# Optimization experiments

Hardware: AMD Instinct MI355X
Metric: run time of the kernel (lower is better)

## Reference

```python
import jax, jax.numpy as jnp
import numpy as np

F_TOT = 108
OUT_CH = 5
GNN_IN = 5


def setup_inputs() -> dict:
    key = jax.random.key(0)
    ks = jax.random.split(key, 24)
    B, S, N, E = 16, 1, 20000, 320000
    s = 0.1  # param init scale
    d = {}
    d["x"] = jax.random.normal(ks[0], (B, S, N, F_TOT), jnp.float32)
    d["edge_index"] = jax.random.randint(ks[1], (2, E), 0, N, dtype=jnp.int32)
    # four Conv1d(1, 5, k=24) branches
    for i, nm in enumerate(["t", "r", "tp", "ssr"]):
        d[f"w_{nm}"] = s * jax.random.normal(ks[2 + 2 * i], (OUT_CH, 1, 24), jnp.float32)
        d[f"b_{nm}"] = s * jax.random.normal(ks[3 + 2 * i], (OUT_CH,), jnp.float32)
    # fc1: 32 -> 20, fc2: 20 -> 5
    d["fc1_w"] = s * jax.random.normal(ks[10], (20, 12 + 4 * OUT_CH), jnp.float32)
    d["fc1_b"] = s * jax.random.normal(ks[11], (20,), jnp.float32)
    d["fc2_w"] = s * jax.random.normal(ks[12], (GNN_IN, 20), jnp.float32)
    d["fc2_b"] = s * jax.random.normal(ks[13], (GNN_IN,), jnp.float32)
    # SAGEConv(5 -> 20): lin_l (with bias, applied to mean-aggregated neighbors), lin_r (no bias, root)
    d["g1_wl"] = s * jax.random.normal(ks[14], (20, GNN_IN), jnp.float32)
    d["g1_bl"] = s * jax.random.normal(ks[15], (20,), jnp.float32)
    d["g1_wr"] = s * jax.random.normal(ks[16], (20, GNN_IN), jnp.float32)
    # SAGEConv(20 -> 1)
    d["g2_wl"] = s * jax.random.normal(ks[17], (1, 20), jnp.float32)
    d["g2_bl"] = s * jax.random.normal(ks[18], (1,), jnp.float32)
    d["g2_wr"] = s * jax.random.normal(ks[19], (1, 20), jnp.float32)
    return d


def _branch(xs, w, b):
    # Conv1d(in=1, out=5, k=24) over a length-24 window == a single dot product per channel.
    # xs: [NB, 24], w: [5, 1, 24] -> [NB, 5], then ReLU
    return jax.nn.relu(jnp.einsum('nk,ok->no', xs, w[:, 0, :]) + b)


def _sage(h, src, dst, wl, bl, wr, n_nodes):
    # PyG SAGEConv with mean aggregation: out = lin_l(mean_{j in N(i)} x_j) + lin_r(x_i)
    # h: [B, N, d]
    msg = jnp.transpose(h[:, src, :], (1, 0, 2))                    # [E, B, d]
    agg = jax.ops.segment_sum(msg, dst, num_segments=n_nodes)       # [N, B, d]
    deg = jax.ops.segment_sum(jnp.ones((src.shape[0],), h.dtype), dst, num_segments=n_nodes)
    mean = jnp.transpose(agg, (1, 0, 2)) / jnp.maximum(deg, 1.0)[None, :, None]  # [B, N, d]
    return mean @ wl.T + bl + h @ wr.T


def reference(x, edge_index, w_t, b_t, w_r, b_r, w_tp, b_tp, w_ssr, b_ssr,
              fc1_w, fc1_b, fc2_w, fc2_b, g1_wl, g1_bl, g1_wr, g2_wl, g2_bl, g2_wr):
    B, S, N, F = x.shape
    src, dst = edge_index[0], edge_index[1]
    # permute(2,0,1,3).reshape(N*B, S, F); S == 1
    xs = jnp.transpose(x, (2, 0, 1, 3)).reshape(N * B, S, F)[:, 0, :]  # [NB, 108]
    out_t = _branch(xs[:, 12:36], w_t, b_t)
    out_r = _branch(xs[:, 36:60], w_r, b_r)
    out_tp = _branch(xs[:, 60:84], w_tp, b_tp)
    out_ssr = _branch(xs[:, 84:108], w_ssr, b_ssr)
    feat = jnp.concatenate([xs[:, :12], out_t, out_r, out_tp, out_ssr], axis=1)  # [NB, 32]
    h = jax.nn.relu(feat @ fc1_w.T + fc1_b) @ fc2_w.T + fc2_b                    # [NB, 5]
    h = jnp.transpose(h.reshape(N, B, -1), (1, 0, 2))                            # [B, N, 5]
    h = _sage(h, src, dst, g1_wl, g1_bl, g1_wr, N)                               # [B, N, 20]
    h = _sage(h, src, dst, g2_wl, g2_bl, g2_wr, N)                               # [B, N, 1]
    return jnp.transpose(h, (0, 2, 1))                                           # [B, 1, N]
```

## Files before the change

kernel.cpp:

```cpp
#include <hip/hip_runtime.h>


#define F1W 500
#define F1B 1160
#define CO  1180
#define FEAT 1266
#define HL   3378

__global__ void k_zero(int* __restrict__ cnt, int N) {
  int n = blockIdx.x * blockDim.x + threadIdx.x;
  if (n < N) cnt[n] = 0;
}

__global__ void k_count(const int* __restrict__ dst, int E, int* __restrict__ cnt) {
  int e = blockIdx.x * blockDim.x + threadIdx.x;
  if (e < E) atomicAdd(&cnt[dst[e]], 1);
}

__global__ __launch_bounds__(1024) void k_scan(
    const int* __restrict__ cnt, int N,
    int* __restrict__ row_ptr, int* __restrict__ cursor,
    const float* __restrict__ f2w, const float* __restrict__ f2b,
    const float* __restrict__ g1_wl, const float* __restrict__ g1_bl,
    const float* __restrict__ g1_wr, const float* __restrict__ g2_wl,
    const float* __restrict__ g2_wr, float* __restrict__ coef) {
  int t = threadIdx.x;

  if (t < 21) {
    float a[5], r1[5], c[5], r2[5];
#pragma unroll
    for (int k = 0; k < 5; ++k) { a[k] = 0.f; r1[k] = 0.f; c[k] = 0.f; r2[k] = 0.f; }
#pragma unroll
    for (int j = 0; j < 20; ++j) {
      float wl2 = g2_wl[j], wr2 = g2_wr[j];
#pragma unroll
      for (int k = 0; k < 5; ++k) {
        float wl1 = g1_wl[j * 5 + k], wr1 = g1_wr[j * 5 + k];
        a[k]  = fmaf(wl2, wl1, a[k]);
        r1[k] = fmaf(wr2, wl1, r1[k]);
        c[k]  = fmaf(wl2, wr1, c[k]);
        r2[k] = fmaf(wr2, wr1, r2[k]);
      }
    }
    if (t < 20) {
      float A = 0.f, R1 = 0.f, C = 0.f, R2 = 0.f;
#pragma unroll
      for (int k = 0; k < 5; ++k) {
        float w = f2w[k * 20 + t];
        A  = fmaf(a[k],  w, A);
        R1 = fmaf(r1[k], w, R1);
        C  = fmaf(c[k],  w, C);
        R2 = fmaf(r2[k], w, R2);
      }
      coef[t] = A; coef[20 + t] = R1; coef[40 + t] = C; coef[60 + t] = R2;
    } else {
      float ca = 0.f, cr1 = 0.f, cc = 0.f, cr2 = 0.f;
#pragma unroll
      for (int k = 0; k < 5; ++k) {
        float b = f2b[k];
        ca = fmaf(a[k], b, ca);  cr1 = fmaf(r1[k], b, cr1);
        cc = fmaf(c[k], b, cc);  cr2 = fmaf(r2[k], b, cr2);
      }
      coef[80] = ca; coef[81] = cr1; coef[82] = cc; coef[83] = cr2;
      float kb1 = 0.f, kb2 = 0.f;
#pragma unroll
      for (int j = 0; j < 20; ++j) {
        kb1 = fmaf(g2_wl[j], g1_bl[j], kb1);
        kb2 = fmaf(g2_wr[j], g1_bl[j], kb2);
      }
      coef[84] = kb1; coef[85] = kb2;
    }
  }

  __shared__ int part[1024];
  int chunk = (N + 1023) / 1024;
  int s0 = t * chunk, s1 = min(N, s0 + chunk);
  int sum = 0;
  for (int i = s0; i < s1; ++i) sum += cnt[i];
  part[t] = sum;
  __syncthreads();
  for (int off = 1; off < 1024; off <<= 1) {
    int v = (t >= off) ? part[t - off] : 0;
    __syncthreads();
    part[t] += v;
    __syncthreads();
  }
  int run = (t == 0) ? 0 : part[t - 1];
  for (int i = s0; i < s1; ++i) {
    row_ptr[i] = run; cursor[i] = run;
    run += cnt[i];
  }
  if (s1 == N) row_ptr[N] = run;
}

__global__ void k_scatter(const int* __restrict__ src, const int* __restrict__ dst, int E,
                          int* __restrict__ cursor, int* __restrict__ adj) {
  int e = blockIdx.x * blockDim.x + threadIdx.x;
  if (e < E) {
    int pos = atomicAdd(&cursor[dst[e]], 1);
    adj[pos] = src[e];
  }
}

__global__ __launch_bounds__(256) void k_mlp(
    const float* __restrict__ x,
    const float* __restrict__ w_t, const float* __restrict__ b_t,
    const float* __restrict__ w_r, const float* __restrict__ b_r,
    const float* __restrict__ w_tp, const float* __restrict__ b_tp,
    const float* __restrict__ w_ssr, const float* __restrict__ b_ssr,
    const float* __restrict__ f1w, const float* __restrict__ f1b,
    const float* __restrict__ coef,
    float2* __restrict__ F1v, float2* __restrict__ F2v, int N, int rows) {
  __shared__ float S[4978];
  const int t = threadIdx.x;
  const int q = t & 3, r = t >> 2;
  int rr = blockIdx.x * 64 + r;
  bool live = rr < rows;
  if (!live) rr = rows - 1;

  const float4* xv = reinterpret_cast<const float4*>(x + (size_t)rr * 108);
  float4 bv[6];
#pragma unroll
  for (int i = 0; i < 6; ++i) bv[i] = xv[3 + 6 * q + i];
  float4 pv = make_float4(0.f, 0.f, 0.f, 0.f);
  if (q > 0) pv = xv[q - 1];

  if (t < 120) {
    S[t] = w_t[t]; S[120 + t] = w_r[t]; S[240 + t] = w_tp[t]; S[360 + t] = w_ssr[t];
  }
  if (t < 5) {
    S[480 + t] = b_t[t]; S[485 + t] = b_r[t];
    S[490 + t] = b_tp[t]; S[495 + t] = b_ssr[t];
  }
  for (int i = t; i < 640; i += 256) {
    int o = i >> 5, k = i & 31;
    S[F1W + o * 33 + k] = f1w[i];
  }
  if (t < 20) S[F1B + t] = f1b[t];
  if (t >= 128 && t < 128 + 86) S[CO + t - 128] = coef[t - 128];
  __syncthreads();

  float acc[5];
#pragma unroll
  for (int o = 0; o < 5; ++o) acc[o] = S[480 + q * 5 + o];
#pragma unroll
  for (int i = 0; i < 6; ++i) {
    float4 w4 = bv[i];
#pragma unroll
    for (int o = 0; o < 5; ++o) {
      const int wb = q * 120 + o * 24 + 4 * i;
      acc[o] = fmaf(w4.x, S[wb + 0], acc[o]);
      acc[o] = fmaf(w4.y, S[wb + 1], acc[o]);
      acc[o] = fmaf(w4.z, S[wb + 2], acc[o]);
      acc[o] = fmaf(w4.w, S[wb + 3], acc[o]);
    }
  }
  float* fr = &S[FEAT + r * 33];
  if (q > 0) {
    fr[4 * (q - 1) + 0] = pv.x; fr[4 * (q - 1) + 1] = pv.y;
    fr[4 * (q - 1) + 2] = pv.z; fr[4 * (q - 1) + 3] = pv.w;
  }
#pragma unroll
  for (int o = 0; o < 5; ++o) fr[12 + q * 5 + o] = fmaxf(acc[o], 0.f);
  __syncthreads();

  float a2[5];
#pragma unroll
  for (int j = 0; j < 5; ++j) a2[j] = S[F1B + q * 5 + j];
#pragma unroll
  for (int i = 0; i < 32; ++i) {
    float f = fr[i];
#pragma unroll
    for (int j = 0; j < 5; ++j)
      a2[j] = fmaf(f, S[F1W + (q * 5 + j) * 33 + i], a2[j]);
  }
  float* hr = &S[HL + r * 25];
#pragma unroll
  for (int j = 0; j < 5; ++j) hr[q * 5 + j] = fmaxf(a2[j], 0.f);
  __syncthreads();

  float s = S[CO + 80 + q];
#pragma unroll
  for (int i = 0; i < 20; ++i) s = fmaf(hr[i], S[CO + q * 20 + i], s);
  hr[20 + q] = s;
  __syncthreads();

  if (q == 0 && live) {
    int b = rr / N;
    int n = rr - b * N;
    F1v[n * 16 + b] = make_float2(hr[20], hr[21]);
    F2v[n * 16 + b] = make_float2(hr[22], hr[23]);
  }
}

__global__ void k_agg1(const int* __restrict__ row_ptr, const int* __restrict__ adj,
                       const float2* __restrict__ F1v, const float2* __restrict__ F2v,
                       float* __restrict__ W, float* __restrict__ V, int N) {
  int t = blockIdx.x * blockDim.x + threadIdx.x;
  int g = t >> 4, b = t & 15;
  if (g >= N) return;
  int beg = row_ptr[g], end = row_ptr[g + 1];
  float sa = 0.f, sb = 0.f;
  for (int c = beg; c < end; c += 16) {
    int idx = c + b;
    int a = adj[idx < end ? idx : end - 1];
    int m = min(16, end - c);
    for (int k = 0; k < m; ++k) {
      int s = __shfl(a, k, 16);
      float2 f = F1v[s * 16 + b];
      sa += f.x; sb += f.y;
    }
  }
  float inv = 1.0f / fmaxf((float)(end - beg), 1.0f);
  float2 f2 = F2v[t];
  W[t] = sa * inv + f2.x;
  V[t] = sb * inv;
}

__global__ __launch_bounds__(256) void k_agg2(
    const int* __restrict__ row_ptr, const int* __restrict__ adj,
    const float* __restrict__ W, const float* __restrict__ V,
    const float2* __restrict__ F2v, const float* __restrict__ coef,
    const float* __restrict__ g2_bl, float* __restrict__ out, int N) {
  __shared__ float tile[16][17];
  int t = blockIdx.x * 256 + threadIdx.x;
  int g = t >> 4, b = t & 15;
  float r = 0.f;
  if (g < N) {
    int beg = row_ptr[g], end = row_ptr[g + 1];
    float sw = 0.f;
    for (int c = beg; c < end; c += 16) {
      int idx = c + b;
      int a = adj[idx < end ? idx : end - 1];
      int m = min(16, end - c);
      for (int k = 0; k < m; ++k) {
        int s = __shfl(a, k, 16);
        sw += W[s * 16 + b];
      }
    }
    int deg = end - beg;
    float inv = 1.0f / fmaxf((float)deg, 1.0f);
    float chi = deg > 0 ? 1.f : 0.f;
    r = sw * inv + V[t] + F2v[t].y + coef[84] * chi + coef[85] + g2_bl[0];
  }
  int gl = (threadIdx.x >> 4);
  tile[b][gl] = r;
  __syncthreads();
  int b2 = threadIdx.x >> 4;
  int gl2 = threadIdx.x & 15;
  int n2 = blockIdx.x * 16 + gl2;
  if (n2 < N) out[(size_t)b2 * N + n2] = tile[b2][gl2];
}

extern "C" void kernel_launch(void* const* d_in, const int* in_sizes, int n_in,
                              void* d_out, int out_size, void* d_ws, size_t ws_size,
                              hipStream_t stream) {
  const float* x     = (const float*)d_in[0];
  const int*   ei    = (const int*)d_in[1];
  const float* w_t   = (const float*)d_in[2];
  const float* b_t   = (const float*)d_in[3];
  const float* w_r   = (const float*)d_in[4];
  const float* b_r   = (const float*)d_in[5];
  const float* w_tp  = (const float*)d_in[6];
  const float* b_tp  = (const float*)d_in[7];
  const float* w_ssr = (const float*)d_in[8];
  const float* b_ssr = (const float*)d_in[9];
  const float* f1w   = (const float*)d_in[10];
  const float* f1b   = (const float*)d_in[11];
  const float* f2w   = (const float*)d_in[12];
  const float* f2b   = (const float*)d_in[13];
  const float* g1_wl = (const float*)d_in[14];
  const float* g1_bl = (const float*)d_in[15];
  const float* g1_wr = (const float*)d_in[16];
  const float* g2_wl = (const float*)d_in[17];
  const float* g2_bl = (const float*)d_in[18];
  const float* g2_wr = (const float*)d_in[19];
  float* out = (float*)d_out;

  const int E = in_sizes[1] / 2;
  const int N = out_size / 16;
  const int rows = out_size;
  const int* src = ei;
  const int* dst = ei + E;

  float* ws  = (float*)d_ws;
  float2* F1v = (float2*)ws;
  float2* F2v = F1v + (size_t)16 * N;
  float*  W   = (float*)(F2v + (size_t)16 * N);
  float*  V   = W + (size_t)16 * N;
  float*  coef = V + (size_t)16 * N;
  int* cnt     = (int*)(coef + 128);
  int* row_ptr = cnt + N;
  int* cursor  = row_ptr + N + 1;
  int* adj     = cursor + N;

  int nb16 = (N * 16 + 255) / 256;

  k_zero<<<(N + 255) / 256, 256, 0, stream>>>(cnt, N);
  k_count<<<(E + 255) / 256, 256, 0, stream>>>(dst, E, cnt);
  k_scan<<<1, 1024, 0, stream>>>(cnt, N, row_ptr, cursor,
                                 f2w, f2b, g1_wl, g1_bl, g1_wr, g2_wl, g2_wr, coef);
  k_scatter<<<(E + 255) / 256, 256, 0, stream>>>(src, dst, E, cursor, adj);
  k_mlp<<<(rows + 63) / 64, 256, 0, stream>>>(
      x, w_t, b_t, w_r, b_r, w_tp, b_tp, w_ssr, b_ssr,
      f1w, f1b, coef, F1v, F2v, N, rows);
  k_agg1<<<nb16, 256, 0, stream>>>(row_ptr, adj, F1v, F2v, W, V, N);
  k_agg2<<<nb16, 256, 0, stream>>>(row_ptr, adj, W, V, F2v, coef, g2_bl, out, N);
}
```

Baseline: 145.5 us.

## Double-buffer x tiles into LDS via async global_load_lds in k_mlp

New measurement: 172.7 us. 1.19x slower.

```diff
diff --git a/kernel.cpp b/kernel.cpp
--- a/kernel.cpp
+++ b/kernel.cpp
@@ -1,11 +1,12 @@
 #include <hip/hip_runtime.h>
 
 
-#define F1W 500
-#define F1B 1160
-#define CO  1180
-#define FEAT 1266
-#define HL   3378
+#define BUF0 0
+#define BUF1 6912
+#define WB   13824
+#define FEAT 15090
+#define HL   17202
+#define LDS_TOT 18802
 
 __global__ void k_zero(int* __restrict__ cnt, int N) {
   int n = blockIdx.x * blockDim.x + threadIdx.x;
@@ -102,6 +103,23 @@
   }
 }
 
+__device__ __forceinline__ void stage_tile(const float* __restrict__ x,
+                                           float* lbuf, int row0, int rows,
+                                           int w, int lane) {
+#pragma unroll
+  for (int j = 0; j < 7; ++j) {
+    int s = j * 4 + w; if (s > 26) s = 26;
+    int c = s * 64 + lane;
+    int dr = c / 27, part = c - dr * 27;
+    int row = row0 + dr; if (row >= rows) row = rows - 1;
+    const float* src = x + (size_t)row * 108 + part * 4;
+    __builtin_amdgcn_global_load_lds(
+        (const __attribute__((address_space(1))) unsigned int*)src,
+        (__attribute__((address_space(3))) unsigned int*)(lbuf + s * 256),
+        16, 0, 0);
+  }
+}
+
 __global__ __launch_bounds__(256) void k_mlp(
     const float* __restrict__ x,
     const float* __restrict__ w_t, const float* __restrict__ b_t,
@@ -111,85 +129,103 @@
     const float* __restrict__ f1w, const float* __restrict__ f1b,
     const float* __restrict__ coef,
     float2* __restrict__ F1v, float2* __restrict__ F2v, int N, int rows) {
-  __shared__ float S[4978];
+  __shared__ float S[LDS_TOT];
   const int t = threadIdx.x;
+  const int w = t >> 6, lane = t & 63;
   const int q = t & 3, r = t >> 2;
-  int rr = blockIdx.x * 64 + r;
-  bool live = rr < rows;
-  if (!live) rr = rows - 1;
-
-  const float4* xv = reinterpret_cast<const float4*>(x + (size_t)rr * 108);
-  float4 bv[6];
-#pragma unroll
-  for (int i = 0; i < 6; ++i) bv[i] = xv[3 + 6 * q + i];
-  float4 pv = make_float4(0.f, 0.f, 0.f, 0.f);
-  if (q > 0) pv = xv[q - 1];
+  const int base = blockIdx.x * 256;
+
+  stage_tile(x, S + BUF0, base, rows, w, lane);
 
   if (t < 120) {
-    S[t] = w_t[t]; S[120 + t] = w_r[t]; S[240 + t] = w_tp[t]; S[360 + t] = w_ssr[t];
+    S[WB + t] = w_t[t]; S[WB + 120 + t] = w_r[t];
+    S[WB + 240 + t] = w_tp[t]; S[WB + 360 + t] = w_ssr[t];
   }
   if (t < 5) {
-    S[480 + t] = b_t[t]; S[485 + t] = b_r[t];
-    S[490 + t] = b_tp[t]; S[495 + t] = b_ssr[t];
+    S[WB + 480 + t] = b_t[t]; S[WB + 485 + t] = b_r[t];
+    S[WB + 490 + t] = b_tp[t]; S[WB + 495 + t] = b_ssr[t];
   }
   for (int i = t; i < 640; i += 256) {
     int o = i >> 5, k = i & 31;
-    S[F1W + o * 33 + k] = f1w[i];
-  }
-  if (t < 20) S[F1B + t] = f1b[t];
-  if (t >= 128 && t < 128 + 86) S[CO + t - 128] = coef[t - 128];
-  __syncthreads();
-
-  float acc[5];
-#pragma unroll
-  for (int o = 0; o < 5; ++o) acc[o] = S[480 + q * 5 + o];
-#pragma unroll
-  for (int i = 0; i < 6; ++i) {
-    float4 w4 = bv[i];
-#pragma unroll
-    for (int o = 0; o < 5; ++o) {
-      const int wb = q * 120 + o * 24 + 4 * i;
-      acc[o] = fmaf(w4.x, S[wb + 0], acc[o]);
-      acc[o] = fmaf(w4.y, S[wb + 1], acc[o]);
-      acc[o] = fmaf(w4.z, S[wb + 2], acc[o]);
-      acc[o] = fmaf(w4.w, S[wb + 3], acc[o]);
-    }
-  }
-  float* fr = &S[FEAT + r * 33];
-  if (q > 0) {
-    fr[4 * (q - 1) + 0] = pv.x; fr[4 * (q - 1) + 1] = pv.y;
-    fr[4 * (q - 1) + 2] = pv.z; fr[4 * (q - 1) + 3] = pv.w;
-  }
-#pragma unroll
-  for (int o = 0; o < 5; ++o) fr[12 + q * 5 + o] = fmaxf(acc[o], 0.f);
-  __syncthreads();
-
-  float a2[5];
-#pragma unroll
-  for (int j = 0; j < 5; ++j) a2[j] = S[F1B + q * 5 + j];
-#pragma unroll
-  for (int i = 0; i < 32; ++i) {
-    float f = fr[i];
-#pragma unroll
-    for (int j = 0; j < 5; ++j)
-      a2[j] = fmaf(f, S[F1W + (q * 5 + j) * 33 + i], a2[j]);
-  }
-  float* hr = &S[HL + r * 25];
-#pragma unroll
-  for (int j = 0; j < 5; ++j) hr[q * 5 + j] = fmaxf(a2[j], 0.f);
-  __syncthreads();
-
-  float s = S[CO + 80 + q];
-#pragma unroll
-  for (int i = 0; i < 20; ++i) s = fmaf(hr[i], S[CO + q * 20 + i], s);
-  hr[20 + q] = s;
-  __syncthreads();
-
-  if (q == 0 && live) {
-    int b = rr / N;
-    int n = rr - b * N;
-    F1v[n * 16 + b] = make_float2(hr[20], hr[21]);
-    F2v[n * 16 + b] = make_float2(hr[22], hr[23]);
+    S[WB + 500 + o * 33 + k] = f1w[i];
+  }
+  if (t < 20) S[WB + 1160 + t] = f1b[t];
+  if (t >= 128 && t < 128 + 86) S[WB + 1180 + t - 128] = coef[t - 128];
+
+  for (int st = 0; st < 4; ++st) {
+    float* cur = S + ((st & 1) ? BUF1 : BUF0);
+    if (st < 3) {
+      stage_tile(x, S + ((st & 1) ? BUF0 : BUF1), base + (st + 1) * 64, rows, w, lane);
+      asm volatile("s_waitcnt vmcnt(7) lgkmcnt(0)" ::: "memory");
+    } else {
+      asm volatile("s_waitcnt vmcnt(0) lgkmcnt(0)" ::: "memory");
+    }
+    __builtin_amdgcn_sched_barrier(0);
+    __builtin_amdgcn_s_barrier();
+    __builtin_amdgcn_sched_barrier(0);
+
+    int rr = base + st * 64 + r;
+    bool live = rr < rows;
+    const float* xr = cur + r * 108;
+
+    float acc[5];
+#pragma unroll
+    for (int o = 0; o < 5; ++o) acc[o] = S[WB + 480 + q * 5 + o];
+#pragma unroll
+    for (int i = 0; i < 6; ++i) {
+      float4 w4 = *reinterpret_cast<const float4*>(xr + 12 + 24 * q + 4 * i);
+#pragma unroll
+      for (int o = 0; o < 5; ++o) {
+        const int wb = WB + q * 120 + o * 24 + 4 * i;
+        acc[o] = fmaf(w4.x, S[wb + 0], acc[o]);
+        acc[o] = fmaf(w4.y, S[wb + 1], acc[o]);
+        acc[o] = fmaf(w4.z, S[wb + 2], acc[o]);
+        acc[o] = fmaf(w4.w, S[wb + 3], acc[o]);
+      }
+    }
+    float* fr = &S[FEAT + r * 33];
+    if (q > 0) {
+      float4 pv = *reinterpret_cast<const float4*>(xr + 4 * (q - 1));
+      fr[4 * (q - 1) + 0] = pv.x; fr[4 * (q - 1) + 1] = pv.y;
+      fr[4 * (q - 1) + 2] = pv.z; fr[4 * (q - 1) + 3] = pv.w;
+    }
+#pragma unroll
+    for (int o = 0; o < 5; ++o) fr[12 + q * 5 + o] = fmaxf(acc[o], 0.f);
+    asm volatile("s_waitcnt lgkmcnt(0)" ::: "memory");
+    __builtin_amdgcn_s_barrier();
+    __builtin_amdgcn_sched_barrier(0);
+
+    float a2[5];
+#pragma unroll
+    for (int j = 0; j < 5; ++j) a2[j] = S[WB + 1160 + q * 5 + j];
+#pragma unroll
+    for (int i = 0; i < 32; ++i) {
+      float f = fr[i];
+#pragma unroll
+      for (int j = 0; j < 5; ++j)
+        a2[j] = fmaf(f, S[WB + 500 + (q * 5 + j) * 33 + i], a2[j]);
+    }
+    float* hr = &S[HL + r * 25];
+#pragma unroll
+    for (int j = 0; j < 5; ++j) hr[q * 5 + j] = fmaxf(a2[j], 0.f);
+    asm volatile("s_waitcnt lgkmcnt(0)" ::: "memory");
+    __builtin_amdgcn_s_barrier();
+    __builtin_amdgcn_sched_barrier(0);
+
+    float s = S[WB + 1180 + 80 + q];
+#pragma unroll
+    for (int i = 0; i < 20; ++i) s = fmaf(hr[i], S[WB + 1180 + q * 20 + i], s);
+    hr[20 + q] = s;
+    asm volatile("s_waitcnt lgkmcnt(0)" ::: "memory");
+    __builtin_amdgcn_s_barrier();
+    __builtin_amdgcn_sched_barrier(0);
+
+    if (q == 0 && live) {
+      int b = rr / N;
+      int n = rr - b * N;
+      F1v[n * 16 + b] = make_float2(hr[20], hr[21]);
+      F2v[n * 16 + b] = make_float2(hr[22], hr[23]);
+    }
   }
 }
 
@@ -301,7 +337,7 @@
   k_scan<<<1, 1024, 0, stream>>>(cnt, N, row_ptr, cursor,
                                  f2w, f2b, g1_wl, g1_bl, g1_wr, g2_wl, g2_wr, coef);
   k_scatter<<<(E + 255) / 256, 256, 0, stream>>>(src, dst, E, cursor, adj);
-  k_mlp<<<(rows + 63) / 64, 256, 0, stream>>>(
+  k_mlp<<<(rows + 255) / 256, 256, 0, stream>>>(
       x, w_t, b_t, w_r, b_r, w_tp, b_tp, w_ssr, b_ssr,
       f1w, f1b, coef, F1v, F2v, N, rows);
   k_agg1<<<nb16, 256, 0, stream>>>(row_ptr, adj, F1v, F2v, W, V, N);
```
